# Optimization experiments

Measured on AMD Instinct MI355X. Metric: run time of the kernel, lower is better.

Reference implementation:

```python
import jax, jax.numpy as jnp
import numpy as np

HID = 256; NH = 8; DH = 32; NL = 2
NV = 20000; NT = 50000; NE = 100000; NC = 8; FIN = 64


def setup_inputs() -> dict:
    ks = jax.random.split(jax.random.key(0), 32)
    f = lambda i, sh, s: jax.random.normal(ks[i], sh, dtype=jnp.float32) * s
    return {
        "x_v": f(0, (NV, FIN), 1.0),
        "x_t": f(1, (NT, FIN), 1.0),
        "ei_vt_src": jax.random.randint(ks[2], (NE,), 0, NV),
        "ei_vt_dst": jax.random.randint(ks[3], (NE,), 0, NT),
        "ei_tv_src": jax.random.randint(ks[4], (NE,), 0, NT),
        "ei_tv_dst": jax.random.randint(ks[5], (NE,), 0, NV),
        "ei_tt_src": jax.random.randint(ks[6], (NE,), 0, NT),
        "ei_tt_dst": jax.random.randint(ks[7], (NE,), 0, NT),
        "current": jax.random.randint(ks[8], (NC, 2), 0, NV),
        "W_in_v": f(9, (FIN, HID), 0.05), "b_in_v": jnp.zeros((HID,)),
        "W_in_t": f(10, (FIN, HID), 0.05), "b_in_t": jnp.zeros((HID,)),
        "Wk": f(11, (NL, 2, HID, HID), 0.05), "bk": jnp.zeros((NL, 2, HID)),
        "Wq": f(12, (NL, 2, HID, HID), 0.05), "bq": jnp.zeros((NL, 2, HID)),
        "Wv": f(13, (NL, 2, HID, HID), 0.05), "bv": jnp.zeros((NL, 2, HID)),
        "Wa": f(14, (NL, 2, HID, HID), 0.05), "ba": jnp.zeros((NL, 2, HID)),
        "skip": jnp.zeros((NL, 2)),
        "a_rel": f(15, (NL, 3, NH, DH, DH), 0.1),
        "m_rel": f(16, (NL, 3, NH, DH, DH), 0.1),
        "p_rel": jnp.ones((NL, 3, NH)),
        "Ws1": f(17, (2 * HID, HID), 0.05), "bs1": jnp.zeros((HID,)),
        "Ws2": f(18, (HID, 2), 0.05), "bs2": jnp.zeros((2,)),
    }


def reference(x_v, x_t, ei_vt_src, ei_vt_dst, ei_tv_src, ei_tv_dst,
              ei_tt_src, ei_tt_dst, current,
              W_in_v, b_in_v, W_in_t, b_in_t,
              Wk, bk, Wq, bq, Wv, bv, Wa, ba, skip,
              a_rel, m_rel, p_rel, Ws1, bs1, Ws2, bs2):
    scale = 1.0 / jnp.sqrt(jnp.float32(DH))
    # input projections + relu (lin_dict)
    hv = jax.nn.relu(x_v @ W_in_v + b_in_v)
    ht = jax.nn.relu(x_t @ W_in_t + b_in_t)
    # edge types: (src_type, dst_type, rel_idx, src_idx, dst_idx); 0=vehicle, 1=track
    edges = [(0, 1, 0, ei_vt_src, ei_vt_dst),
             (1, 0, 1, ei_tv_src, ei_tv_dst),
             (1, 1, 2, ei_tt_src, ei_tt_dst)]
    for l in range(NL):
        h = (hv, ht)
        proj = lambda W, b, t: (h[t] @ W[l, t] + b[l, t]).reshape(-1, NH, DH)
        k = (proj(Wk, bk, 0), proj(Wk, bk, 1))
        q = (proj(Wq, bq, 0), proj(Wq, bq, 1))
        v = (proj(Wv, bv, 0), proj(Wv, bv, 1))
        agg = [jnp.zeros((NV, NH, DH), jnp.float32),
               jnp.zeros((NT, NH, DH), jnp.float32)]
        for (st, dt, r, si, di) in edges:
            nd = agg[dt].shape[0]
            ke = jnp.einsum('ehd,hdf->ehf', k[st][si], a_rel[l, r])  # [E,H,D]
            ve = jnp.einsum('ehd,hdf->ehf', v[st][si], m_rel[l, r])  # [E,H,D]
            logit = (q[dt][di] * ke).sum(-1) * p_rel[l, r] * scale    # [E,H]
            m = jax.ops.segment_max(logit, di, num_segments=nd)
            e = jnp.exp(logit - m[di])
            s = jax.ops.segment_sum(e, di, num_segments=nd)
            alpha = e / (s[di] + 1e-16)
            agg[dt] = agg[dt] + jax.ops.segment_sum(alpha[..., None] * ve, di,
                                                    num_segments=nd)
        new = []
        for t in (0, 1):
            o = jax.nn.gelu(agg[t].reshape(-1, HID), approximate=False) @ Wa[l, t] + ba[l, t]
            beta = jax.nn.sigmoid(skip[l, t])
            new.append(beta * o + (1.0 - beta) * h[t])
        hv, ht = new
    # batched Scorer over (current vehicles) x (all tracks); cat([track, vehicle])
    veh = hv[current[:, 0]]                 # [C,HID]
    tpart = ht @ Ws1[:HID]                  # [NT,HID]
    vpart = veh @ Ws1[HID:] + bs1           # [C,HID]
    hmid = jax.nn.relu(tpart[None, :, :] + vpart[:, None, :])  # [C,NT,HID]
    out = hmid @ Ws2 + bs2                  # [C,NT,2]
    return out[..., 0], jax.nn.sigmoid(out[..., 1])
```

## Files before the change

kernel.cpp:

```cpp
#include <hip/hip_runtime.h>
#include <hip/hip_bf16.h>
#include <math.h>

#define HID 256
#define NH 8
#define DH 32
#define NL 2
#define NV 20000
#define NT 50000
#define NE 100000
#define NC 8
#define FIN 64

typedef unsigned short u16;
typedef unsigned int u32;
typedef short s16x8 __attribute__((ext_vector_type(8)));
typedef float f32x4 __attribute__((ext_vector_type(4)));

__device__ __forceinline__ float bf2f(u16 u) { return __uint_as_float(((u32)u) << 16); }
__device__ __forceinline__ u16 f2bf(float f) {
    u32 x = __float_as_uint(f);
    u32 r = ((x >> 16) & 1u) + 0x7fffu;
    return (u16)((x + r) >> 16);
}
__device__ __forceinline__ void up2(u32 u, float& a, float& b) {
    a = __uint_as_float(u << 16);
    b = __uint_as_float(u & 0xffff0000u);
}
__device__ __forceinline__ s16x8 gelu8(s16x8 a) {
    s16x8 r;
#pragma unroll
    for (int i = 0; i < 8; i++) {
        float v = bf2f((u16)a[i]);
        v = 0.5f * v * (1.f + erff(v * 0.70710678118654752f));
        r[i] = (short)f2bf(v);
    }
    return r;
}

__global__ void k_zero_i(int* __restrict__ p, int n) {
    for (int i = blockIdx.x * 256 + threadIdx.x; i < n; i += gridDim.x * 256) p[i] = 0;
}

__global__ void k_hist(const int* __restrict__ dst, int* __restrict__ cnt) {
    for (int e = blockIdx.x * 256 + threadIdx.x; e < NE; e += gridDim.x * 256)
        atomicAdd(&cnt[dst[e]], 1);
}

__global__ __launch_bounds__(1024) void k_scan(const int* __restrict__ cnt, int* __restrict__ rp, int n) {
    __shared__ int wsum[16];
    __shared__ int carry_s;
    int t = threadIdx.x, lane = t & 63, wv = t >> 6;
    if (t == 0) { carry_s = 0; rp[0] = 0; }
    __syncthreads();
    for (int base = 0; base < n; base += 1024) {
        int v = (base + t < n) ? cnt[base + t] : 0;
        int x = v;
#pragma unroll
        for (int off = 1; off < 64; off <<= 1) {
            int y = __shfl_up(x, off, 64);
            if (lane >= off) x += y;
        }
        if (lane == 63) wsum[wv] = x;
        __syncthreads();
        if (wv == 0 && lane < 16) {
            int s = wsum[lane];
#pragma unroll
            for (int off = 1; off < 16; off <<= 1) {
                int y = __shfl_up(s, off, 64);
                if (lane >= off) s += y;
            }
            wsum[lane] = s;
        }
        __syncthreads();
        int prefix = carry_s + (wv > 0 ? wsum[wv - 1] : 0);
        if (base + t < n) rp[base + t + 1] = prefix + x;
        __syncthreads();
        if (t == 0) carry_s += wsum[15];
        __syncthreads();
    }
}

__global__ void k_copy_i(const int* __restrict__ a, int* __restrict__ b, int n) {
    for (int i = blockIdx.x * 256 + threadIdx.x; i < n; i += gridDim.x * 256) b[i] = a[i];
}

__global__ void k_scatter(const int* __restrict__ dst, const int* __restrict__ src,
                          int* __restrict__ fill, int* __restrict__ es) {
    for (int e = blockIdx.x * 256 + threadIdx.x; e < NE; e += gridDim.x * 256) {
        int d = dst[e];
        int p = atomicAdd(&fill[d], 1);
        es[p] = src[e];
    }
}

__global__ __launch_bounds__(256) void k_in_proj(const float* __restrict__ X, const float* __restrict__ W,
                          const float* __restrict__ b, u16* __restrict__ Y, int N) {
    const int NPB = 16;
    __shared__ float xs[NPB][FIN];
    int n0 = blockIdx.x * NPB;
    int t = threadIdx.x;
    for (int idx = t; idx < NPB * FIN; idx += 256) {
        int i = idx >> 6, c = idx & 63;
        int n = n0 + i;
        xs[i][c] = (n < N) ? X[(size_t)n * FIN + c] : 0.f;
    }
    __syncthreads();
    float acc[NPB];
#pragma unroll
    for (int i = 0; i < NPB; i++) acc[i] = 0.f;
    for (int c = 0; c < FIN; c++) {
        float w = W[c * HID + t];
#pragma unroll
        for (int i = 0; i < NPB; i++) acc[i] += xs[i][c] * w;
    }
    float bb = b[t];
    for (int i = 0; i < NPB; i++) {
        int n = n0 + i;
        if (n < N) Y[(size_t)n * HID + t] = f2bf(fmaxf(acc[i] + bb, 0.f));
    }
}

__device__ __forceinline__ int swz_idx(int k, int n) {
    int ks = k >> 5, r = k & 31;
    int j = r & 7;
    int l = ((r >> 3) << 4) | (n & 15);
    int nt = n >> 4;
    return ((ks * 16 + nt) * 64 + l) * 8 + j;
}

__global__ __launch_bounds__(256) void k_fuse_w(const float* __restrict__ W, const float* __restrict__ b,
                        const float* __restrict__ R, u16* __restrict__ Wsw, float* __restrict__ bout) {
    int h = blockIdx.x;
    __shared__ float sR[DH * DH];
    int t = threadIdx.x;
    for (int idx = t; idx < DH * DH; idx += 256) sR[idx] = R[h * DH * DH + idx];
    __syncthreads();
    int f = t & 31, c0 = t >> 5;
    for (int c = c0; c < HID; c += 8) {
        float acc = 0.f;
#pragma unroll
        for (int d = 0; d < DH; d++) acc += W[c * HID + h * DH + d] * sR[d * DH + f];
        Wsw[swz_idx(c, h * DH + f)] = f2bf(acc);
    }
    if (t < DH) {
        float acc = 0.f;
#pragma unroll
        for (int d = 0; d < DH; d++) acc += b[h * DH + d] * sR[d * DH + t];
        bout[h * DH + t] = acc;
    }
}

__global__ __launch_bounds__(256) void k_swz_multi(const float* __restrict__ Wq, const float* __restrict__ Wa,
                                                   const float* __restrict__ Ws1, u16* __restrict__ out) {
    int slot = blockIdx.x >> 8;
    int idx = ((blockIdx.x & 255) << 8) | threadIdx.x;
    const float* src = (slot < 4) ? (Wq + (size_t)slot * 65536)
                     : (slot < 8) ? (Wa + (size_t)(slot - 4) * 65536)
                                  : Ws1;
    int j = idx & 7, l = (idx >> 3) & 63, nt = (idx >> 9) & 15, ks = idx >> 13;
    int k = ks * 32 + (l >> 4) * 8 + j;
    int n = nt * 16 + (l & 15);
    out[(size_t)slot * 65536 + idx] = f2bf(src[k * HID + n]);
}

template <int MODE, int GELU>
__global__ __launch_bounds__(256) void k_mm(const u16* __restrict__ X, const u16* __restrict__ Wsw,
                                            const float* __restrict__ bias, void* __restrict__ Y,
                                            const float* __restrict__ skip_, int N) {
    int tid = threadIdx.x;
    int w = tid >> 6, lane = tid & 63;
    int r0 = blockIdx.x * 16;
    int rA = r0 + (lane & 15);
    int koffg = lane >> 4;
    s16x8 a[8];
    if (rA < N) {
        const s16x8* ap = (const s16x8*)(X + (size_t)rA * HID) + koffg;
#pragma unroll
        for (int ks = 0; ks < 8; ks++) a[ks] = ap[ks * 4];
    } else {
#pragma unroll
        for (int ks = 0; ks < 8; ks++) a[ks] = (s16x8){0, 0, 0, 0, 0, 0, 0, 0};
    }
    if (GELU) {
#pragma unroll
        for (int ks = 0; ks < 8; ks++) a[ks] = gelu8(a[ks]);
    }
    f32x4 acc[4];
#pragma unroll
    for (int nt = 0; nt < 4; nt++) acc[nt] = (f32x4){0.f, 0.f, 0.f, 0.f};
    const s16x8* wp = (const s16x8*)Wsw;
#pragma unroll
    for (int ks = 0; ks < 8; ks++) {
        const s16x8* wq = wp + (size_t)ks * 16 * 64 + lane;
#pragma unroll
        for (int nt = 0; nt < 4; nt++) {
            s16x8 b = wq[(w * 4 + nt) * 64];
            acc[nt] = __builtin_amdgcn_mfma_f32_16x16x32_bf16(a[ks], b, acc[nt], 0, 0, 0);
        }
    }
    int colb = lane & 15;
    int rowb = r0 + koffg * 4;
    float beta = 0.f, ombeta = 0.f;
    if (MODE == 2) { beta = 1.f / (1.f + expf(-skip_[0])); ombeta = 1.f - beta; }
#pragma unroll
    for (int nt = 0; nt < 4; nt++) {
        int col = w * 64 + nt * 16 + colb;
        float bb = (MODE == 1) ? 0.f : bias[col];
#pragma unroll
        for (int j = 0; j < 4; j++) {
            int row = rowb + j;
            if (row < N) {
                float v = acc[nt][j] + bb;
                if (MODE == 0) {
                    ((u16*)Y)[(size_t)row * HID + col] = f2bf(v);
                } else if (MODE == 1) {
                    ((float*)Y)[(size_t)row * HID + col] = v;
                } else {
                    u16* hp = (u16*)Y + (size_t)row * HID + col;
                    *hp = f2bf(beta * v + ombeta * bf2f(*hp));
                }
            }
        }
    }
}

__global__ __launch_bounds__(256) void k_mm2(const u16* __restrict__ X,
                                             const u16* __restrict__ W1, const float* __restrict__ b1, u16* __restrict__ Y1,
                                             const u16* __restrict__ W2, const float* __restrict__ b2, u16* __restrict__ Y2,
                                             int N) {
    int tid = threadIdx.x;
    int w = tid >> 6, lane = tid & 63;
    int r0 = blockIdx.x * 16;
    int rA = r0 + (lane & 15);
    int koffg = lane >> 4;
    s16x8 a[8];
    if (rA < N) {
        const s16x8* ap = (const s16x8*)(X + (size_t)rA * HID) + koffg;
#pragma unroll
        for (int ks = 0; ks < 8; ks++) a[ks] = ap[ks * 4];
    } else {
#pragma unroll
        for (int ks = 0; ks < 8; ks++) a[ks] = (s16x8){0, 0, 0, 0, 0, 0, 0, 0};
    }
    int colb = lane & 15;
    int rowb = r0 + koffg * 4;
#pragma unroll
    for (int pass = 0; pass < 2; pass++) {
        const u16* Wsw = pass ? W2 : W1;
        const float* bias = pass ? b2 : b1;
        u16* Y = pass ? Y2 : Y1;
        f32x4 acc[4];
#pragma unroll
        for (int nt = 0; nt < 4; nt++) acc[nt] = (f32x4){0.f, 0.f, 0.f, 0.f};
        const s16x8* wp = (const s16x8*)Wsw;
#pragma unroll
        for (int ks = 0; ks < 8; ks++) {
            const s16x8* wq = wp + (size_t)ks * 16 * 64 + lane;
#pragma unroll
            for (int nt = 0; nt < 4; nt++) {
                s16x8 b = wq[(w * 4 + nt) * 64];
                acc[nt] = __builtin_amdgcn_mfma_f32_16x16x32_bf16(a[ks], b, acc[nt], 0, 0, 0);
            }
        }
#pragma unroll
        for (int nt = 0; nt < 4; nt++) {
            int col = w * 64 + nt * 16 + colb;
            float bb = bias[col];
#pragma unroll
            for (int j = 0; j < 4; j++) {
                int row = rowb + j;
                if (row < N) Y[(size_t)row * HID + col] = f2bf(acc[nt][j] + bb);
            }
        }
    }
}

__global__ __launch_bounds__(256) void k_mm3(const u16* __restrict__ X,
                                             const u16* __restrict__ W0, const float* __restrict__ b0, u16* __restrict__ Y0,
                                             const u16* __restrict__ W1, const float* __restrict__ b1, u16* __restrict__ Y1,
                                             const u16* __restrict__ W2, const float* __restrict__ b2, u16* __restrict__ Y2,
                                             int N) {
    int tid = threadIdx.x;
    int w = tid >> 6, lane = tid & 63;
    int r0 = blockIdx.x * 16;
    int rA = r0 + (lane & 15);
    int koffg = lane >> 4;
    s16x8 a[8];
    if (rA < N) {
        const s16x8* ap = (const s16x8*)(X + (size_t)rA * HID) + koffg;
#pragma unroll
        for (int ks = 0; ks < 8; ks++) a[ks] = ap[ks * 4];
    } else {
#pragma unroll
        for (int ks = 0; ks < 8; ks++) a[ks] = (s16x8){0, 0, 0, 0, 0, 0, 0, 0};
    }
    int colb = lane & 15;
    int rowb = r0 + koffg * 4;
#pragma unroll
    for (int pass = 0; pass < 3; pass++) {
        const u16* Wsw = (pass == 0) ? W0 : (pass == 1) ? W1 : W2;
        const float* bias = (pass == 0) ? b0 : (pass == 1) ? b1 : b2;
        u16* Y = (pass == 0) ? Y0 : (pass == 1) ? Y1 : Y2;
        f32x4 acc[4];
#pragma unroll
        for (int nt = 0; nt < 4; nt++) acc[nt] = (f32x4){0.f, 0.f, 0.f, 0.f};
        const s16x8* wp = (const s16x8*)Wsw;
#pragma unroll
        for (int ks = 0; ks < 8; ks++) {
            const s16x8* wq = wp + (size_t)ks * 16 * 64 + lane;
#pragma unroll
            for (int nt = 0; nt < 4; nt++) {
                s16x8 b = wq[(w * 4 + nt) * 64];
                acc[nt] = __builtin_amdgcn_mfma_f32_16x16x32_bf16(a[ks], b, acc[nt], 0, 0, 0);
            }
        }
#pragma unroll
        for (int nt = 0; nt < 4; nt++) {
            int col = w * 64 + nt * 16 + colb;
            float bb = bias[col];
#pragma unroll
            for (int j = 0; j < 4; j++) {
                int row = rowb + j;
                if (row < N) Y[(size_t)row * HID + col] = f2bf(acc[nt][j] + bb);
            }
        }
    }
}

__device__ __forceinline__ void attn_pass(const u16* __restrict__ kA, const u16* __restrict__ vM,
                                          const int* __restrict__ es, int jb, int je,
                                          float q0, float q1, float q2, float q3, float ph, int lane4,
                                          float& o0, float& o1, float& o2, float& o3) {
    float m = -INFINITY, ss = 0.f, a0 = 0.f, a1 = 0.f, a2 = 0.f, a3 = 0.f;
    uint2 kuN = {0, 0}, vuN = {0, 0};
    if (jb < je) {
        int s0 = es[jb];
        kuN = *(const uint2*)(kA + (size_t)s0 * HID + lane4);
        vuN = *(const uint2*)(vM + (size_t)s0 * HID + lane4);
    }
    for (int j = jb; j < je; j++) {
        uint2 ku = kuN, vu = vuN;
        if (j + 1 < je) {
            int s1 = es[j + 1];
            kuN = *(const uint2*)(kA + (size_t)s1 * HID + lane4);
            vuN = *(const uint2*)(vM + (size_t)s1 * HID + lane4);
        }
        float k0, k1, k2, k3; up2(ku.x, k0, k1); up2(ku.y, k2, k3);
        float part = q0 * k0 + q1 * k1 + q2 * k2 + q3 * k3;
        part += __shfl_xor(part, 1, 64);
        part += __shfl_xor(part, 2, 64);
        part += __shfl_xor(part, 4, 64);
        float logit = part * ph;
        float nm = fmaxf(m, logit);
        float corr = expf(m - nm);
        float ee = expf(logit - nm);
        float v0, v1, v2, v3; up2(vu.x, v0, v1); up2(vu.y, v2, v3);
        ss = ss * corr + ee;
        a0 = a0 * corr + ee * v0; a1 = a1 * corr + ee * v1;
        a2 = a2 * corr + ee * v2; a3 = a3 * corr + ee * v3;
        m = nm;
    }
    float inv = 1.f / (ss + 1e-16f);
    o0 += a0 * inv; o1 += a1 * inv; o2 += a2 * inv; o3 += a3 * inv;
}

__global__ __launch_bounds__(256) void k_node_attn(
        const u16* __restrict__ q, const u16* __restrict__ kA, const u16* __restrict__ vM,
        const int* __restrict__ rp, const int* __restrict__ es,
        const float* __restrict__ P, float scale,
        u16* __restrict__ agg, int Nd) {
    int node = blockIdx.x * 4 + (threadIdx.x >> 6);
    if (node >= Nd) return;
    int lane = threadIdx.x & 63;
    float ph = P[lane >> 3] * scale;
    uint2 qu = *(const uint2*)(q + (size_t)node * HID + lane * 4);
    float q0, q1, q2, q3; up2(qu.x, q0, q1); up2(qu.y, q2, q3);
    float o0 = 0.f, o1 = 0.f, o2 = 0.f, o3 = 0.f;
    attn_pass(kA, vM, es, rp[node], rp[node + 1], q0, q1, q2, q3, ph, lane * 4, o0, o1, o2, o3);
    u16* ap = agg + (size_t)node * HID + lane * 4;
    ap[0] = f2bf(o0); ap[1] = f2bf(o1); ap[2] = f2bf(o2); ap[3] = f2bf(o3);
}

__global__ __launch_bounds__(256) void k_node_attn2(
        const u16* __restrict__ q,
        const u16* __restrict__ kA0, const u16* __restrict__ vM0,
        const int* __restrict__ rp0, const int* __restrict__ es0, const float* __restrict__ P0,
        const u16* __restrict__ kA1, const u16* __restrict__ vM1,
        const int* __restrict__ rp1, const int* __restrict__ es1, const float* __restrict__ P1,
        float scale, u16* __restrict__ agg, int Nd) {
    int node = blockIdx.x * 4 + (threadIdx.x >> 6);
    if (node >= Nd) return;
    int lane = threadIdx.x & 63;
    int h = lane >> 3;
    float ph0 = P0[h] * scale, ph1 = P1[h] * scale;
    uint2 qu = *(const uint2*)(q + (size_t)node * HID + lane * 4);
    float q0, q1, q2, q3; up2(qu.x, q0, q1); up2(qu.y, q2, q3);
    float o0 = 0.f, o1 = 0.f, o2 = 0.f, o3 = 0.f;
    attn_pass(kA0, vM0, es0, rp0[node], rp0[node + 1], q0, q1, q2, q3, ph0, lane * 4, o0, o1, o2, o3);
    attn_pass(kA1, vM1, es1, rp1[node], rp1[node + 1], q0, q1, q2, q3, ph1, lane * 4, o0, o1, o2, o3);
    u16* ap = agg + (size_t)node * HID + lane * 4;
    ap[0] = f2bf(o0); ap[1] = f2bf(o1); ap[2] = f2bf(o2); ap[3] = f2bf(o3);
}

__global__ void k_vpart(const u16* __restrict__ hv, const int* __restrict__ current,
                        const float* __restrict__ Ws1, const float* __restrict__ bs1,
                        float* __restrict__ vpart) {
    __shared__ float row[HID];
    int t = threadIdx.x;
    for (int c = 0; c < NC; c++) {
        int n = current[c * 2];
        row[t] = bf2f(hv[(size_t)n * HID + t]);
        __syncthreads();
        float acc = 0.f;
        for (int i = 0; i < HID; i++) acc += row[i] * Ws1[(size_t)(HID + i) * HID + t];
        vpart[c * HID + t] = acc + bs1[t];
        __syncthreads();
    }
}

__global__ __launch_bounds__(256) void k_final(const float* __restrict__ tpart, const float* __restrict__ vpart,
                        const float* __restrict__ Ws2, const float* __restrict__ bs2,
                        float* __restrict__ out) {
    __shared__ float vp[NC * HID];
    int t = threadIdx.x;
    for (int idx = t; idx < NC * HID; idx += 256) vp[idx] = vpart[idx];
    __syncthreads();
    int lane = t & 63, w = t >> 6;
    float w20[4], w21[4];
#pragma unroll
    for (int i = 0; i < 4; i++) {
        w20[i] = Ws2[(lane + 64 * i) * 2 + 0];
        w21[i] = Ws2[(lane + 64 * i) * 2 + 1];
    }
    float b0 = bs2[0], b1 = bs2[1];
    for (int n = blockIdx.x * 4 + w; n < NT; n += gridDim.x * 4) {
        float tp[4];
#pragma unroll
        for (int i = 0; i < 4; i++) tp[i] = tpart[(size_t)n * HID + lane + 64 * i];
#pragma unroll
        for (int c = 0; c < NC; c++) {
            float a0 = 0.f, a1 = 0.f;
#pragma unroll
            for (int i = 0; i < 4; i++) {
                float hm = fmaxf(tp[i] + vp[c * HID + lane + 64 * i], 0.f);
                a0 += hm * w20[i];
                a1 += hm * w21[i];
            }
#pragma unroll
            for (int off = 32; off >= 1; off >>= 1) {
                a0 += __shfl_xor(a0, off, 64);
                a1 += __shfl_xor(a1, off, 64);
            }
            if (lane == 0) {
                out[(size_t)c * NT + n] = a0 + b0;
                float z = a1 + b1;
                out[(size_t)NC * NT + (size_t)c * NT + n] = 1.f / (1.f + expf(-z));
            }
        }
    }
}

extern "C" void kernel_launch(void* const* d_in, const int* in_sizes, int n_in,
                              void* d_out, int out_size, void* d_ws, size_t ws_size,
                              hipStream_t stream) {
    (void)in_sizes; (void)n_in; (void)out_size;
    const float* x_v    = (const float*)d_in[0];
    const float* x_t    = (const float*)d_in[1];
    const int* ei_vt_s  = (const int*)d_in[2];
    const int* ei_vt_d  = (const int*)d_in[3];
    const int* ei_tv_s  = (const int*)d_in[4];
    const int* ei_tv_d  = (const int*)d_in[5];
    const int* ei_tt_s  = (const int*)d_in[6];
    const int* ei_tt_d  = (const int*)d_in[7];
    const int* current  = (const int*)d_in[8];
    const float* W_in_v = (const float*)d_in[9];
    const float* b_in_v = (const float*)d_in[10];
    const float* W_in_t = (const float*)d_in[11];
    const float* b_in_t = (const float*)d_in[12];
    const float* Wk     = (const float*)d_in[13];
    const float* bk     = (const float*)d_in[14];
    const float* Wq     = (const float*)d_in[15];
    const float* bq     = (const float*)d_in[16];
    const float* Wv     = (const float*)d_in[17];
    const float* bv     = (const float*)d_in[18];
    const float* Wa     = (const float*)d_in[19];
    const float* ba     = (const float*)d_in[20];
    const float* skip   = (const float*)d_in[21];
    const float* a_rel  = (const float*)d_in[22];
    const float* m_rel  = (const float*)d_in[23];
    const float* p_rel  = (const float*)d_in[24];
    const float* Ws1    = (const float*)d_in[25];
    const float* bs1    = (const float*)d_in[26];
    const float* Ws2    = (const float*)d_in[27];
    const float* bs2    = (const float*)d_in[28];

    char* p = (char*)d_ws;
    auto alloc = [&](size_t bytes) -> char* {
        char* r = p;
        p += (bytes + 255) & ~(size_t)255;
        return r;
    };
    u16* hv   = (u16*)alloc((size_t)NV * HID * 2);
    u16* ht   = (u16*)alloc((size_t)NT * HID * 2);
    u16* qb   = (u16*)alloc((size_t)NT * HID * 2);
    u16* qv   = (u16*)alloc((size_t)NV * HID * 2);
    u16* kA   = (u16*)alloc((size_t)NT * HID * 2);
    u16* vM   = (u16*)alloc((size_t)NT * HID * 2);
    u16* kA0  = (u16*)alloc((size_t)NV * HID * 2);
    u16* vM0  = (u16*)alloc((size_t)NV * HID * 2);
    u16* agg  = (u16*)alloc((size_t)NT * HID * 2);
    int* rp_vt = (int*)alloc((size_t)(NT + 1) * 4);
    int* rp_tv = (int*)alloc((size_t)(NV + 1) * 4);
    int* rp_tt = (int*)alloc((size_t)(NT + 1) * 4);
    int* es_vt = (int*)alloc((size_t)NE * 4);
    int* es_tv = (int*)alloc((size_t)NE * 4);
    int* es_tt = (int*)alloc((size_t)NE * 4);
    int* cnt   = (int*)alloc((size_t)NT * 4);
    int* fill  = (int*)alloc((size_t)NT * 4);
    float* vp  = (float*)alloc((size_t)NC * HID * 4);
    float* bkF = (float*)alloc(HID * 4);
    float* bvF = (float*)alloc(HID * 4);
    u16*  wswK = (u16*)alloc((size_t)HID * HID * 2);
    u16*  wswV = (u16*)alloc((size_t)HID * HID * 2);
    u16*  wswK2 = (u16*)alloc((size_t)HID * HID * 2);
    u16*  wswV2 = (u16*)alloc((size_t)HID * HID * 2);
    float* bkF2 = (float*)alloc(HID * 4);
    float* bvF2 = (float*)alloc(HID * 4);
    u16*  wswA = (u16*)alloc((size_t)9 * HID * HID * 2);
    if ((size_t)(p - (char*)d_ws) > ws_size) return;

    const float scale = 0.17677669529663687f;

    {
        const int* DL[3] = { ei_vt_d, ei_tv_d, ei_tt_d };
        const int* SL[3] = { ei_vt_s, ei_tv_s, ei_tt_s };
        int* RP[3] = { rp_vt, rp_tv, rp_tt };
        int* ES[3] = { es_vt, es_tv, es_tt };
        int ND[3] = { NT, NV, NT };
        for (int r = 0; r < 3; r++) {
            k_zero_i<<<256, 256, 0, stream>>>(cnt, ND[r]);
            k_hist<<<512, 256, 0, stream>>>(DL[r], cnt);
            k_scan<<<1, 1024, 0, stream>>>(cnt, RP[r], ND[r]);
            k_copy_i<<<256, 256, 0, stream>>>(RP[r], fill, ND[r]);
            k_scatter<<<512, 256, 0, stream>>>(DL[r], SL[r], fill, ES[r]);
        }
    }

    k_swz_multi<<<9 * 256, 256, 0, stream>>>(Wq, Wa, Ws1, wswA);

    k_in_proj<<<(NV + 15) / 16, 256, 0, stream>>>(x_v, W_in_v, b_in_v, hv, NV);
    k_in_proj<<<(NT + 15) / 16, 256, 0, stream>>>(x_t, W_in_t, b_in_t, ht, NT);

    const int GV = (NV + 15) / 16, GT = (NT + 15) / 16;

    for (int l = 0; l < NL; l++) {
        const float* Wk0 = Wk + (size_t)(l * 2 + 0) * HID * HID;
        const float* Wk1 = Wk + (size_t)(l * 2 + 1) * HID * HID;
        const float* bk0 = bk + (l * 2 + 0) * HID, *bk1 = bk + (l * 2 + 1) * HID;
        const float* Wv0 = Wv + (size_t)(l * 2 + 0) * HID * HID;
        const float* Wv1 = Wv + (size_t)(l * 2 + 1) * HID * HID;
        const float* bv0 = bv + (l * 2 + 0) * HID, *bv1 = bv + (l * 2 + 1) * HID;
        const float* bq0 = bq + (l * 2 + 0) * HID, *bq1 = bq + (l * 2 + 1) * HID;
        const u16* WqS0 = wswA + (size_t)(l * 2 + 0) * 65536;
        const u16* WqS1 = wswA + (size_t)(l * 2 + 1) * 65536;
        const u16* WaS0 = wswA + (size_t)(4 + l * 2 + 0) * 65536;
        const u16* WaS1 = wswA + (size_t)(4 + l * 2 + 1) * 65536;
        const float* A0 = a_rel + (size_t)(l * 3 + 0) * NH * DH * DH;
        const float* A1 = a_rel + (size_t)(l * 3 + 1) * NH * DH * DH;
        const float* A2 = a_rel + (size_t)(l * 3 + 2) * NH * DH * DH;
        const float* M0 = m_rel + (size_t)(l * 3 + 0) * NH * DH * DH;
        const float* M1 = m_rel + (size_t)(l * 3 + 1) * NH * DH * DH;
        const float* M2 = m_rel + (size_t)(l * 3 + 2) * NH * DH * DH;
        const float* P0 = p_rel + (size_t)(l * 3 + 0) * NH;
        const float* P1 = p_rel + (size_t)(l * 3 + 1) * NH;
        const float* P2 = p_rel + (size_t)(l * 3 + 2) * NH;

        k_fuse_w<<<NH, 256, 0, stream>>>(Wk0, bk0, A0, wswK, bkF);
        k_fuse_w<<<NH, 256, 0, stream>>>(Wv0, bv0, M0, wswV, bvF);
        k_mm3<<<GV, 256, 0, stream>>>(hv, WqS0, bq0, qv, wswK, bkF, kA0, wswV, bvF, vM0, NV);

        k_fuse_w<<<NH, 256, 0, stream>>>(Wk1, bk1, A1, wswK, bkF);
        k_fuse_w<<<NH, 256, 0, stream>>>(Wv1, bv1, M1, wswV, bvF);
        k_mm3<<<GT, 256, 0, stream>>>(ht, WqS1, bq1, qb, wswK, bkF, kA, wswV, bvF, vM, NT);

        k_node_attn<<<(NV + 3) / 4, 256, 0, stream>>>(qv, kA, vM, rp_tv, es_tv, P1, scale, agg, NV);

        k_mm<2, 1><<<GV, 256, 0, stream>>>(agg, WaS0, ba + (l * 2 + 0) * HID, hv, skip + (l * 2 + 0), NV);

        k_fuse_w<<<NH, 256, 0, stream>>>(Wk1, bk1, A2, wswK2, bkF2);
        k_fuse_w<<<NH, 256, 0, stream>>>(Wv1, bv1, M2, wswV2, bvF2);
        k_mm2<<<GT, 256, 0, stream>>>(ht, wswK2, bkF2, kA, wswV2, bvF2, vM, NT);

        k_node_attn2<<<(NT + 3) / 4, 256, 0, stream>>>(qb, kA0, vM0, rp_vt, es_vt, P0,
                                                       kA, vM, rp_tt, es_tt, P2, scale, agg, NT);

        k_mm<2, 1><<<GT, 256, 0, stream>>>(agg, WaS1, ba + (l * 2 + 1) * HID, ht, skip + (l * 2 + 1), NT);
    }

    k_vpart<<<1, 256, 0, stream>>>(hv, current, Ws1, bs1, vp);
    float* tpart = (float*)kA;
    k_mm<1, 0><<<GT, 256, 0, stream>>>(ht, wswA + (size_t)8 * 65536, nullptr, (void*)tpart, nullptr, NT);
    k_final<<<2048, 256, 0, stream>>>(tpart, vp, Ws2, bs2, (float*)d_out);
}
```

Baseline: 1.177 ms.

## Batch CSR build across relations and store tpart in bf16

```diff
diff --git a/kernel.cpp b/kernel.cpp
--- a/kernel.cpp
+++ b/kernel.cpp
@@ -42,12 +42,22 @@
     for (int i = blockIdx.x * 256 + threadIdx.x; i < n; i += gridDim.x * 256) p[i] = 0;
 }
 
-__global__ void k_hist(const int* __restrict__ dst, int* __restrict__ cnt) {
-    for (int e = blockIdx.x * 256 + threadIdx.x; e < NE; e += gridDim.x * 256)
+__global__ void k_hist3(const int* __restrict__ d0, const int* __restrict__ d1, const int* __restrict__ d2,
+                        int* __restrict__ cnt3) {
+    int r = blockIdx.x >> 9;
+    int b = blockIdx.x & 511;
+    const int* dst = (r == 0) ? d0 : (r == 1) ? d1 : d2;
+    int* cnt = cnt3 + (size_t)r * NT;
+    for (int e = b * 256 + threadIdx.x; e < NE; e += 512 * 256)
         atomicAdd(&cnt[dst[e]], 1);
 }
 
-__global__ __launch_bounds__(1024) void k_scan(const int* __restrict__ cnt, int* __restrict__ rp, int n) {
+__global__ __launch_bounds__(1024) void k_scan3(const int* __restrict__ cnt3,
+                                                int* __restrict__ rp0, int* __restrict__ rp1, int* __restrict__ rp2) {
+    int r = blockIdx.x;
+    const int* cnt = cnt3 + (size_t)r * NT;
+    int* rp = (r == 0) ? rp0 : (r == 1) ? rp1 : rp2;
+    int n = (r == 1) ? NV : NT;
     __shared__ int wsum[16];
     __shared__ int carry_s;
     int t = threadIdx.x, lane = t & 63, wv = t >> 6;
@@ -81,13 +91,28 @@
     }
 }
 
-__global__ void k_copy_i(const int* __restrict__ a, int* __restrict__ b, int n) {
-    for (int i = blockIdx.x * 256 + threadIdx.x; i < n; i += gridDim.x * 256) b[i] = a[i];
-}
-
-__global__ void k_scatter(const int* __restrict__ dst, const int* __restrict__ src,
-                          int* __restrict__ fill, int* __restrict__ es) {
-    for (int e = blockIdx.x * 256 + threadIdx.x; e < NE; e += gridDim.x * 256) {
+__global__ void k_copy3(const int* __restrict__ rp0, const int* __restrict__ rp1, const int* __restrict__ rp2,
+                        int* __restrict__ fill3) {
+    int r = blockIdx.x >> 8;
+    int b = blockIdx.x & 255;
+    const int* rp = (r == 0) ? rp0 : (r == 1) ? rp1 : rp2;
+    int n = (r == 1) ? NV : NT;
+    int* fill = fill3 + (size_t)r * NT;
+    for (int i = b * 256 + threadIdx.x; i < n; i += 256 * 256) fill[i] = rp[i];
+}
+
+__global__ void k_scatter3(const int* __restrict__ d0, const int* __restrict__ s0,
+                           const int* __restrict__ d1, const int* __restrict__ s1,
+                           const int* __restrict__ d2, const int* __restrict__ s2,
+                           int* __restrict__ fill3,
+                           int* __restrict__ es0, int* __restrict__ es1, int* __restrict__ es2) {
+    int r = blockIdx.x >> 9;
+    int b = blockIdx.x & 511;
+    const int* dst = (r == 0) ? d0 : (r == 1) ? d1 : d2;
+    const int* src = (r == 0) ? s0 : (r == 1) ? s1 : s2;
+    int* fill = fill3 + (size_t)r * NT;
+    int* es = (r == 0) ? es0 : (r == 1) ? es1 : es2;
+    for (int e = b * 256 + threadIdx.x; e < NE; e += 512 * 256) {
         int d = dst[e];
         int p = atomicAdd(&fill[d], 1);
         es[p] = src[e];
@@ -206,13 +231,13 @@
 #pragma unroll
     for (int nt = 0; nt < 4; nt++) {
         int col = w * 64 + nt * 16 + colb;
-        float bb = (MODE == 1) ? 0.f : bias[col];
+        float bb = (MODE == 1 || MODE == 3) ? 0.f : bias[col];
 #pragma unroll
         for (int j = 0; j < 4; j++) {
             int row = rowb + j;
             if (row < N) {
                 float v = acc[nt][j] + bb;
-                if (MODE == 0) {
+                if (MODE == 0 || MODE == 3) {
                     ((u16*)Y)[(size_t)row * HID + col] = f2bf(v);
                 } else if (MODE == 1) {
                     ((float*)Y)[(size_t)row * HID + col] = v;
@@ -419,7 +444,7 @@
     }
 }
 
-__global__ __launch_bounds__(256) void k_final(const float* __restrict__ tpart, const float* __restrict__ vpart,
+__global__ __launch_bounds__(256) void k_final(const u16* __restrict__ tpart, const float* __restrict__ vpart,
                         const float* __restrict__ Ws2, const float* __restrict__ bs2,
                         float* __restrict__ out) {
     __shared__ float vp[NC * HID];
@@ -437,7 +462,7 @@
     for (int n = blockIdx.x * 4 + w; n < NT; n += gridDim.x * 4) {
         float tp[4];
 #pragma unroll
-        for (int i = 0; i < 4; i++) tp[i] = tpart[(size_t)n * HID + lane + 64 * i];
+        for (int i = 0; i < 4; i++) tp[i] = bf2f(tpart[(size_t)n * HID + lane + 64 * i]);
 #pragma unroll
         for (int c = 0; c < NC; c++) {
             float a0 = 0.f, a1 = 0.f;
@@ -516,8 +541,8 @@
     int* es_vt = (int*)alloc((size_t)NE * 4);
     int* es_tv = (int*)alloc((size_t)NE * 4);
     int* es_tt = (int*)alloc((size_t)NE * 4);
-    int* cnt   = (int*)alloc((size_t)NT * 4);
-    int* fill  = (int*)alloc((size_t)NT * 4);
+    int* cnt3  = (int*)alloc((size_t)3 * NT * 4);
+    int* fill3 = (int*)alloc((size_t)3 * NT * 4);
     float* vp  = (float*)alloc((size_t)NC * HID * 4);
     float* bkF = (float*)alloc(HID * 4);
     float* bvF = (float*)alloc(HID * 4);
@@ -532,20 +557,12 @@
 
     const float scale = 0.17677669529663687f;
 
-    {
-        const int* DL[3] = { ei_vt_d, ei_tv_d, ei_tt_d };
-        const int* SL[3] = { ei_vt_s, ei_tv_s, ei_tt_s };
-        int* RP[3] = { rp_vt, rp_tv, rp_tt };
-        int* ES[3] = { es_vt, es_tv, es_tt };
-        int ND[3] = { NT, NV, NT };
-        for (int r = 0; r < 3; r++) {
-            k_zero_i<<<256, 256, 0, stream>>>(cnt, ND[r]);
-            k_hist<<<512, 256, 0, stream>>>(DL[r], cnt);
-            k_scan<<<1, 1024, 0, stream>>>(cnt, RP[r], ND[r]);
-            k_copy_i<<<256, 256, 0, stream>>>(RP[r], fill, ND[r]);
-            k_scatter<<<512, 256, 0, stream>>>(DL[r], SL[r], fill, ES[r]);
-        }
-    }
+    k_zero_i<<<256, 256, 0, stream>>>(cnt3, 3 * NT);
+    k_hist3<<<3 * 512, 256, 0, stream>>>(ei_vt_d, ei_tv_d, ei_tt_d, cnt3);
+    k_scan3<<<3, 1024, 0, stream>>>(cnt3, rp_vt, rp_tv, rp_tt);
+    k_copy3<<<3 * 256, 256, 0, stream>>>(rp_vt, rp_tv, rp_tt, fill3);
+    k_scatter3<<<3 * 512, 256, 0, stream>>>(ei_vt_d, ei_vt_s, ei_tv_d, ei_tv_s, ei_tt_d, ei_tt_s,
+                                            fill3, es_vt, es_tv, es_tt);
 
     k_swz_multi<<<9 * 256, 256, 0, stream>>>(Wq, Wa, Ws1, wswA);
 
@@ -599,7 +616,7 @@
     }
 
     k_vpart<<<1, 256, 0, stream>>>(hv, current, Ws1, bs1, vp);
-    float* tpart = (float*)kA;
-    k_mm<1, 0><<<GT, 256, 0, stream>>>(ht, wswA + (size_t)8 * 65536, nullptr, (void*)tpart, nullptr, NT);
+    u16* tpart = kA;
+    k_mm<3, 0><<<GT, 256, 0, stream>>>(ht, wswA + (size_t)8 * 65536, nullptr, (void*)tpart, nullptr, NT);
     k_final<<<2048, 256, 0, stream>>>(tpart, vp, Ws2, bs2, (float*)d_out);
 }
```

Result: faster. 1.097 ms (-6.8%).
